# Kernel tuning notes

Measured on AMD Instinct MI355X. Metric: run time of the kernel, lower is better.

## Reference

```python
import jax, jax.numpy as jnp
import numpy as np

RADIUS = 0.2
NSAMPLE = 32
USE_XYZ = True

B, N, S, C = 8, 8192, 2048, 64


def setup_inputs() -> dict:
    key = jax.random.key(0)
    k1, k2, k3 = jax.random.split(key, 3)
    xyz = jax.random.uniform(k1, (B, N, 3), dtype=jnp.float32)
    new_xyz = jax.random.uniform(k2, (B, S, 3), dtype=jnp.float32)
    features = jax.random.normal(k3, (B, N, C), dtype=jnp.float32)
    return {"xyz": xyz, "new_xyz": new_xyz, "features": features}


def _ball_query(new_xyz, xyz, radius, nsample):
    # new_xyz: (B,S,3), xyz: (B,N,3) -> idx (B,S,nsample) int32
    n = xyz.shape[1]
    d2 = jnp.sum((new_xyz[:, :, None, :] - xyz[:, None, :, :]) ** 2, axis=-1)  # (B,S,N)
    mask = d2 < radius * radius
    # keys: index j if inside ball else N (sentinel); smallest nsample keys = first
    # nsample in-ball indices in ascending j order (matches CUDA ball_query order).
    keys = jnp.where(mask, jnp.arange(n, dtype=jnp.int32), jnp.int32(n))
    neg_vals, _ = jax.lax.top_k(-keys, nsample)  # top_k of -keys -> smallest keys
    idx = -neg_vals  # (B,S,nsample), ascending
    first = idx[..., 0:1]
    idx = jnp.where(idx == n, first, idx)   # pad empty slots with first hit
    idx = jnp.where(idx == n, 0, idx)       # balls with zero hits -> index 0
    return idx


def _group(points, idx):
    # points: (B,N,D), idx: (B,S,K) -> (B,S,K,D)
    return jax.vmap(lambda p, i: p[i])(points, idx)


def reference(xyz, new_xyz, features):
    idx = _ball_query(new_xyz, xyz, RADIUS, NSAMPLE)
    grouped_xyz = _group(xyz, idx) - new_xyz[:, :, None, :]  # (B,S,K,3)
    grouped_feat = _group(features, idx)                      # (B,S,K,C)
    if USE_XYZ:
        new_features = jnp.concatenate([grouped_xyz, grouped_feat], axis=-1)
    else:
        new_features = grouped_feat
    return jnp.transpose(new_features, (0, 3, 1, 2))  # (B, C+3, S, K)
```

## Files before the change

kernel.cpp:

```cpp
#include <hip/hip_runtime.h>

#define BB 8
#define NN 8192
#define SS 2048
#define CC 64
#define NS 32
#define COUT 67
#define QT 8
#define PMAX 35

__global__ __launch_bounds__(256) void transpose_kernel(
    const float* __restrict__ xyz,
    float* __restrict__ xs, float* __restrict__ ys, float* __restrict__ zs)
{
    const int t = blockIdx.x * 256 + threadIdx.x;
    const float* p = xyz + (size_t)t * 3;
    xs[t] = p[0];
    ys[t] = p[1];
    zs[t] = p[2];
}

__global__ __launch_bounds__(256) void scan_kernel(
    const float* __restrict__ xs,
    const float* __restrict__ ys,
    const float* __restrict__ zs,
    const float* __restrict__ new_xyz,
    int* __restrict__ idx_ws)
{
#pragma clang fp contract(off)
    const int wave = threadIdx.x >> 6;
    const int lane = threadIdx.x & 63;
    const int qid  = blockIdx.x * 4 + wave;
    const int b = qid >> 11;
    const int s = qid & 2047;

    const float R2 = 0.04f;

    const float* ctr = new_xyz + ((size_t)b * SS + s) * 3;
    const float cx = ctr[0], cy = ctr[1], cz = ctr[2];

    const float2* xb = (const float2*)(xs + (size_t)b * NN);
    const float2* yb = (const float2*)(ys + (size_t)b * NN);
    const float2* zb = (const float2*)(zs + (size_t)b * NN);

    int* myidx = idx_ws + (size_t)qid * NS;
    const unsigned long long lt = (1ull << lane) - 1ull;

    int total = 0;
    int firstIdx = -1;
    for (int j0 = 0; j0 < NN && total < NS; j0 += 512) {
        float2 X[4], Y[4], Z[4];
#pragma unroll
        for (int u = 0; u < 4; ++u) {
            const int i2 = (j0 >> 1) + u * 64 + lane;
            X[u] = xb[i2];
            Y[u] = yb[i2];
            Z[u] = zb[i2];
        }
#pragma unroll
        for (int u = 0; u < 4; ++u) {
            const float dx0 = X[u].x - cx, dx1 = X[u].y - cx;
            const float dy0 = Y[u].x - cy, dy1 = Y[u].y - cy;
            const float dz0 = Z[u].x - cz, dz1 = Z[u].y - cz;
            float d20 = dx0 * dx0;
            float d21 = dx1 * dx1;
            d20 = d20 + dy0 * dy0;
            d21 = d21 + dy1 * dy1;
            d20 = d20 + dz0 * dz0;
            d21 = d21 + dz1 * dz1;
            const bool h0 = d20 < R2;
            const bool h1 = d21 < R2;
            const unsigned long long lo = __ballot(h0);
            const unsigned long long hi = __ballot(h1);
            const int jg = j0 + u * 128;
            if (firstIdx < 0 && (lo | hi)) {
                int cand = 0x7fffffff;
                if (lo) cand = jg + 2 * __builtin_ctzll(lo);
                if (hi) {
                    const int c2 = jg + 2 * __builtin_ctzll(hi) + 1;
                    cand = (c2 < cand) ? c2 : cand;
                }
                firstIdx = cand;
            }
            const int clo = __popcll(lo & lt);
            const int chi = __popcll(hi & lt);
            if (h0) {
                const int pos = total + clo + chi;
                if (pos < NS) myidx[pos] = jg + 2 * lane;
            }
            if (h1) {
                const int pos = total + clo + chi + (h0 ? 1 : 0);
                if (pos < NS) myidx[pos] = jg + 2 * lane + 1;
            }
            total += __popcll(lo) + __popcll(hi);
        }
    }
    if (total < NS) {
        const int fill = (total > 0) ? firstIdx : 0;
        if (lane >= total && lane < NS) myidx[lane] = fill;
    }
}

__global__ __launch_bounds__(256) void gather_kernel(
    const float* __restrict__ xyz,
    const float* __restrict__ new_xyz,
    const float* __restrict__ feat,
    const int* __restrict__ idx_ws,
    float* __restrict__ out)
{
#pragma clang fp contract(off)
    __shared__ float tile[PMAX * QT * NS];
    __shared__ int idx_sh[QT * NS];

    const int t     = threadIdx.x;
    const int sTile = blockIdx.x;
    const int half  = blockIdx.y;
    const int b     = blockIdx.z;

    const int s0 = sTile * QT;
    const int qbase = (b << 11) + s0;

    idx_sh[t] = idx_ws[(size_t)qbase * NS + t];
    __syncthreads();

    const int q = t >> 5;
    const int row = idx_sh[t];

    const float* frow = feat + ((size_t)b * NN + row) * CC + half * 32;
    if (half == 0) {
        const float* ctr = new_xyz + ((size_t)b * SS + s0 + q) * 3;
        const float* p   = xyz + ((size_t)b * NN + row) * 3;
        tile[0 * 256 + t] = p[0] - ctr[0];
        tile[1 * 256 + t] = p[1] - ctr[1];
        tile[2 * 256 + t] = p[2] - ctr[2];
#pragma unroll
        for (int i = 0; i < 8; ++i) {
            const float4 f = *(const float4*)(frow + i * 4);
            tile[(3 + i * 4 + 0) * 256 + t] = f.x;
            tile[(3 + i * 4 + 1) * 256 + t] = f.y;
            tile[(3 + i * 4 + 2) * 256 + t] = f.z;
            tile[(3 + i * 4 + 3) * 256 + t] = f.w;
        }
    } else {
#pragma unroll
        for (int i = 0; i < 8; ++i) {
            const float4 f = *(const float4*)(frow + i * 4);
            tile[(i * 4 + 0) * 256 + t] = f.x;
            tile[(i * 4 + 1) * 256 + t] = f.y;
            tile[(i * 4 + 2) * 256 + t] = f.z;
            tile[(i * 4 + 3) * 256 + t] = f.w;
        }
    }
    __syncthreads();

    const int P     = half ? 32 : PMAX;
    const int cbase = half ? PMAX : 0;
    const int wv = t >> 6;
    const int ln = t & 63;
    const size_t plane = (size_t)SS * NS;
    float* ob = out + (((size_t)b * COUT + cbase) * SS + s0) * NS;
#pragma unroll
    for (int i = 0; i < 9; ++i) {
        const int p = i * 4 + wv;
        if (p < P) {
            const float4 v = *(const float4*)(tile + p * 256 + ln * 4);
            *(float4*)(ob + (size_t)p * plane + ln * 4) = v;
        }
    }
}

extern "C" void kernel_launch(void* const* d_in, const int* in_sizes, int n_in,
                              void* d_out, int out_size, void* d_ws, size_t ws_size,
                              hipStream_t stream) {
    const float* xyz     = (const float*)d_in[0];
    const float* new_xyz = (const float*)d_in[1];
    const float* feat    = (const float*)d_in[2];
    float* out = (float*)d_out;

    int*   idx_ws = (int*)d_ws;
    float* xs = (float*)((char*)d_ws + (size_t)BB * SS * NS * 4);
    float* ys = xs + (size_t)BB * NN;
    float* zs = ys + (size_t)BB * NN;

    transpose_kernel<<<dim3(BB * NN / 256), dim3(256), 0, stream>>>(xyz, xs, ys, zs);
    scan_kernel<<<dim3((BB * SS) / 4), dim3(256), 0, stream>>>(xs, ys, zs, new_xyz, idx_ws);
    gather_kernel<<<dim3(SS / QT, 2, BB), dim3(256), 0, stream>>>(xyz, new_xyz, feat, idx_ws, out);
}
```

Baseline: 197.6 us.

## Split ball-query scan across four waves per query with shared-memory merge

Each query is now handled by a full block whose four waves scan separate quarters of the point cloud in parallel. Each wave collects up to the first 32 hits into shared memory, and a final merge concatenates the strips in order and applies the padding rule. This aims to shorten the serial scan latency per query, but it adds redundant scanning past the early-exit point, a block-wide barrier, and a less-unrolled inner loop.

```diff
diff --git a/kernel.cpp b/kernel.cpp
--- a/kernel.cpp
+++ b/kernel.cpp
@@ -28,9 +28,12 @@
     int* __restrict__ idx_ws)
 {
 #pragma clang fp contract(off)
+    __shared__ int wlist[4][NS];
+    __shared__ int wcount[4];
+
     const int wave = threadIdx.x >> 6;
     const int lane = threadIdx.x & 63;
-    const int qid  = blockIdx.x * 4 + wave;
+    const int qid  = blockIdx.x;
     const int b = qid >> 11;
     const int s = qid & 2047;
 
@@ -43,61 +46,52 @@
     const float2* yb = (const float2*)(ys + (size_t)b * NN);
     const float2* zb = (const float2*)(zs + (size_t)b * NN);
 
-    int* myidx = idx_ws + (size_t)qid * NS;
     const unsigned long long lt = (1ull << lane) - 1ull;
+    const int sbase = wave * 1024;
 
-    int total = 0;
-    int firstIdx = -1;
-    for (int j0 = 0; j0 < NN && total < NS; j0 += 512) {
-        float2 X[4], Y[4], Z[4];
-#pragma unroll
-        for (int u = 0; u < 4; ++u) {
-            const int i2 = (j0 >> 1) + u * 64 + lane;
-            X[u] = xb[i2];
-            Y[u] = yb[i2];
-            Z[u] = zb[i2];
-        }
-#pragma unroll
-        for (int u = 0; u < 4; ++u) {
-            const float dx0 = X[u].x - cx, dx1 = X[u].y - cx;
-            const float dy0 = Y[u].x - cy, dy1 = Y[u].y - cy;
-            const float dz0 = Z[u].x - cz, dz1 = Z[u].y - cz;
-            float d20 = dx0 * dx0;
-            float d21 = dx1 * dx1;
-            d20 = d20 + dy0 * dy0;
-            d21 = d21 + dy1 * dy1;
-            d20 = d20 + dz0 * dz0;
-            d21 = d21 + dz1 * dz1;
-            const bool h0 = d20 < R2;
-            const bool h1 = d21 < R2;
-            const unsigned long long lo = __ballot(h0);
-            const unsigned long long hi = __ballot(h1);
-            const int jg = j0 + u * 128;
-            if (firstIdx < 0 && (lo | hi)) {
-                int cand = 0x7fffffff;
-                if (lo) cand = jg + 2 * __builtin_ctzll(lo);
-                if (hi) {
-                    const int c2 = jg + 2 * __builtin_ctzll(hi) + 1;
-                    cand = (c2 < cand) ? c2 : cand;
-                }
-                firstIdx = cand;
-            }
-            const int clo = __popcll(lo & lt);
-            const int chi = __popcll(hi & lt);
-            if (h0) {
-                const int pos = total + clo + chi;
-                if (pos < NS) myidx[pos] = jg + 2 * lane;
-            }
-            if (h1) {
-                const int pos = total + clo + chi + (h0 ? 1 : 0);
-                if (pos < NS) myidx[pos] = jg + 2 * lane + 1;
-            }
-            total += __popcll(lo) + __popcll(hi);
-        }
+    int tot = 0;
+    for (int g = 0; g < 16 && tot < NS; ++g) {
+        const int i2 = sbase + g * 64 + lane;
+        const float2 X = xb[i2];
+        const float2 Y = yb[i2];
+        const float2 Z = zb[i2];
+        const float dx0 = X.x - cx, dx1 = X.y - cx;
+        const float dy0 = Y.x - cy, dy1 = Y.y - cy;
+        const float dz0 = Z.x - cz, dz1 = Z.y - cz;
+        float d20 = dx0 * dx0;
+        float d21 = dx1 * dx1;
+        d20 = d20 + dy0 * dy0;
+        d21 = d21 + dy1 * dy1;
+        d20 = d20 + dz0 * dz0;
+        d21 = d21 + dz1 * dz1;
+        const bool h0 = d20 < R2;
+        const bool h1 = d21 < R2;
+        const unsigned long long lo = __ballot(h0);
+        const unsigned long long hi = __ballot(h1);
+        const int ce = __popcll(lo & lt) + __popcll(hi & lt);
+        const int pos0 = tot + ce;
+        const int pos1 = pos0 + (h0 ? 1 : 0);
+        if (h0 && pos0 < NS) wlist[wave][pos0] = 2 * i2;
+        if (h1 && pos1 < NS) wlist[wave][pos1] = 2 * i2 + 1;
+        tot += __popcll(lo) + __popcll(hi);
     }
-    if (total < NS) {
-        const int fill = (total > 0) ? firstIdx : 0;
-        if (lane >= total && lane < NS) myidx[lane] = fill;
+    if (lane == 0) wcount[wave] = (tot > NS) ? NS : tot;
+    __syncthreads();
+
+    if (threadIdx.x < NS) {
+        const int k = threadIdx.x;
+        const int c0 = wcount[0], c1 = wcount[1], c2 = wcount[2], c3 = wcount[3];
+        const int p1 = c0, p2 = p1 + c1, p3 = p2 + c2;
+        const int tot4 = p3 + c3;
+        int strip, off;
+        if (k < p1)      { strip = 0; off = k; }
+        else if (k < p2) { strip = 1; off = k - p1; }
+        else if (k < p3) { strip = 2; off = k - p2; }
+        else             { strip = 3; off = k - p3; }
+        const int fstrip = (c0 > 0) ? 0 : (c1 > 0) ? 1 : (c2 > 0) ? 2 : 3;
+        const int fill = (tot4 > 0) ? wlist[fstrip][0] : 0;
+        const int v = (k < tot4) ? wlist[strip][off] : fill;
+        idx_ws[(size_t)qid * NS + k] = v;
     }
 }
 
@@ -183,6 +177,6 @@
     float* zs = ys + (size_t)BB * NN;
 
     transpose_kernel<<<dim3(BB * NN / 256), dim3(256), 0, stream>>>(xyz, xs, ys, zs);
-    scan_kernel<<<dim3((BB * SS) / 4), dim3(256), 0, stream>>>(xs, ys, zs, new_xyz, idx_ws);
+    scan_kernel<<<dim3(BB * SS), dim3(256), 0, stream>>>(xs, ys, zs, new_xyz, idx_ws);
     gather_kernel<<<dim3(SS / QT, 2, BB), dim3(256), 0, stream>>>(xyz, new_xyz, feat, idx_ws, out);
 }
```

After: 232.1 us. +17.4%, slower.
